# Kernel optimization log

Hardware: AMD Instinct MI355X
Metric: run time of the kernel (lower is better)

The kernel has to match this reference:

```python
import jax, jax.numpy as jnp
import numpy as np

NF = 256  # node_feat_size
GF = 256  # graph_feat_size
V = 262144
G = 4096


def setup_inputs() -> dict:
    key = jax.random.key(0)
    ks = jax.random.split(key, 12)
    node_feats = jax.random.normal(ks[0], (V, NF), dtype=jnp.float32)
    g_feats = jax.random.normal(ks[1], (G, GF), dtype=jnp.float32)
    segment_ids = jnp.sort(jax.random.randint(ks[2], (V,), 0, G, dtype=jnp.int32))
    s = 0.05
    # compute_logits: Linear(NF+GF -> 1)
    Wl = jax.random.normal(ks[3], (1, NF + GF), dtype=jnp.float32) * s
    bl = jnp.zeros((1,), dtype=jnp.float32)
    # project_nodes: Linear(NF -> GF)  (dropout=0 -> identity)
    Wp = jax.random.normal(ks[4], (GF, NF), dtype=jnp.float32) * s
    bp = jnp.zeros((GF,), dtype=jnp.float32)
    # GRUCell(GF, GF), torch gate order (r, z, n)
    W_ih = jax.random.normal(ks[5], (3 * GF, GF), dtype=jnp.float32) * s
    W_hh = jax.random.normal(ks[6], (3 * GF, GF), dtype=jnp.float32) * s
    b_ih = jnp.zeros((3 * GF,), dtype=jnp.float32)
    b_hh = jnp.zeros((3 * GF,), dtype=jnp.float32)
    return dict(node_feats=node_feats, g_feats=g_feats, segment_ids=segment_ids,
                Wl=Wl, bl=bl, Wp=Wp, bp=bp,
                W_ih=W_ih, W_hh=W_hh, b_ih=b_ih, b_hh=b_hh)


def reference(node_feats, g_feats, segment_ids, Wl, bl, Wp, bp, W_ih, W_hh, b_ih, b_hh):
    num_graphs = g_feats.shape[0]
    # broadcast relu(g_feats) to nodes, concat with node feats, logits Linear + LeakyReLU
    gb = jax.nn.relu(g_feats)[segment_ids]                      # [V, GF]
    cat = jnp.concatenate([gb, node_feats], axis=1)             # [V, GF+NF]
    z = jax.nn.leaky_relu(cat @ Wl.T + bl, negative_slope=0.01) # [V, 1]
    # segmented softmax over nodes per graph
    m = jax.ops.segment_max(z, segment_ids, num_segments=num_graphs,
                            indices_are_sorted=True)            # [G, 1]
    e = jnp.exp(z - m[segment_ids])                             # [V, 1]
    denom = jax.ops.segment_sum(e, segment_ids, num_segments=num_graphs,
                                indices_are_sorted=True)        # [G, 1]
    a = e / denom[segment_ids]                                  # [V, 1]
    # project nodes (dropout p=0 -> identity) and weighted sum per graph
    hv = node_feats @ Wp.T + bp                                 # [V, GF]
    context = jax.ops.segment_sum(a * hv, segment_ids, num_segments=num_graphs,
                                  indices_are_sorted=True)      # [G, GF]
    context = jax.nn.elu(context)
    # GRUCell: input=context, hidden=g_feats, torch gate order r,z,n
    gi = context @ W_ih.T + b_ih                                # [G, 3*GF]
    gh = g_feats @ W_hh.T + b_hh                                # [G, 3*GF]
    i_r, i_z, i_n = jnp.split(gi, 3, axis=1)
    h_r, h_z, h_n = jnp.split(gh, 3, axis=1)
    r = jax.nn.sigmoid(i_r + h_r)
    u = jax.nn.sigmoid(i_z + h_z)
    n = jnp.tanh(i_n + r * h_n)
    h_new = (1.0 - u) * n + u * g_feats
    return h_new
```

## Files before the change

### kernel.cpp

```cpp
#include <hip/hip_runtime.h>
#include <hip/hip_bf16.h>
#include <stdint.h>

typedef unsigned short u16;
typedef __attribute__((ext_vector_type(8))) short short8;
typedef __attribute__((ext_vector_type(4))) float floatx4;

#define NFEAT 256

__device__ __forceinline__ unsigned short f2b(float f) {
    unsigned int x = __builtin_bit_cast(unsigned int, f);
    x += 0x7fffu + ((x >> 16) & 1u);
    return (unsigned short)(x >> 16);
}
__device__ __forceinline__ float sigmoidf_(float x) {
    return 1.0f / (1.0f + __expf(-x));
}

__global__ void __launch_bounds__(256)
k0_prep(const int* __restrict__ seg, int V, int G, int* __restrict__ off,
        const float* __restrict__ Wp, const float* __restrict__ Wih,
        const float* __restrict__ Whh,
        u16* __restrict__ wpb, u16* __restrict__ wihb, u16* __restrict__ whhb)
{
    const int i = blockIdx.x * 256 + threadIdx.x;

    {
        const int n1 = 256 * 256;
        const int n2 = n1 + 768 * 256;
        const int n3 = n2 + 768 * 256;
        int idx = i * 2;
        if (idx < n3) {
            const float* src; u16* dst; int o;
            if (idx < n1)      { src = Wp;  dst = wpb;  o = idx; }
            else if (idx < n2) { src = Wih; dst = wihb; o = idx - n1; }
            else               { src = Whh; dst = whhb; o = idx - n2; }
            float2 v = *(const float2*)(src + o);
            dst[o]     = f2b(v.x);
            dst[o + 1] = f2b(v.y);
        }
    }

    if (i < V) {
        int s = seg[i];
        int prev = (i == 0) ? -1 : seg[i - 1];
        if (s != prev) {
            for (int g2 = prev + 1; g2 <= s; ++g2) off[g2] = i;
        }
        if (i == V - 1) {
            for (int g2 = s + 1; g2 <= G; ++g2) off[g2] = V;
        }
    }
}

__global__ void __launch_bounds__(256)
k1_attn_pool(const float* __restrict__ nf, const float* __restrict__ gf,
             const int* __restrict__ off, const float* __restrict__ Wl,
             const float* __restrict__ bl,
             u16* __restrict__ s_out,
             float* __restrict__ pres, u16* __restrict__ gfb)
{
    const int g = blockIdx.x;
    const int t = threadIdx.x;
    const int lane = t & 63;
    const int wv = t >> 6;
    __shared__ float red[4];
    __shared__ float accs[4][256];
    __shared__ float lws[4];

    const int start = off[g];
    const int count = off[g + 1] - start;

    const float* base = nf + (size_t)start * NFEAT + lane * 4;
    float4 x[4] = {{0,0,0,0},{0,0,0,0},{0,0,0,0},{0,0,0,0}};
    #pragma unroll
    for (int r = 0; r < 4; ++r) {
        int i = wv * 4 + r;
        if (i < count) x[r] = *(const float4*)(base + (size_t)i * NFEAT);
    }

    const float4 wn = *(const float4*)(Wl + NFEAT + lane * 4);

    const float gfv = gf[(size_t)g * NFEAT + t];
    gfb[(size_t)g * NFEAT + t] = f2b(gfv);
    float v = fmaxf(gfv, 0.0f) * Wl[t];
    #pragma unroll
    for (int o = 32; o > 0; o >>= 1) v += __shfl_xor(v, o);
    if (lane == 0) red[wv] = v;
    __syncthreads();
    const float gbase = (red[0] + red[1]) + (red[2] + red[3]) + bl[0];

    float l = 0.0f;
    float4 acc = {0.f, 0.f, 0.f, 0.f};
    for (int i = wv * 4; i < count; i += 16) {
        float4 nx[4] = {{0,0,0,0},{0,0,0,0},{0,0,0,0},{0,0,0,0}};
        #pragma unroll
        for (int r = 0; r < 4; ++r) {
            if (i + 16 + r < count) nx[r] = *(const float4*)(base + (size_t)(i + 16 + r) * NFEAT);
        }
        float d[4];
        #pragma unroll
        for (int r = 0; r < 4; ++r)
            d[r] = x[r].x * wn.x + x[r].y * wn.y + x[r].z * wn.z + x[r].w * wn.w;
        #pragma unroll
        for (int o = 32; o > 0; o >>= 1) {
            #pragma unroll
            for (int r = 0; r < 4; ++r) d[r] += __shfl_xor(d[r], o);
        }
        #pragma unroll
        for (int r = 0; r < 4; ++r) {
            float z = d[r] + gbase;
            z = (z > 0.0f) ? z : 0.01f * z;
            float p = (i + r < count) ? __expf(z) : 0.0f;
            l += p;
            acc.x += p * x[r].x;
            acc.y += p * x[r].y;
            acc.z += p * x[r].z;
            acc.w += p * x[r].w;
        }
        x[0] = nx[0]; x[1] = nx[1]; x[2] = nx[2]; x[3] = nx[3];
    }

    accs[wv][lane * 4 + 0] = acc.x;
    accs[wv][lane * 4 + 1] = acc.y;
    accs[wv][lane * 4 + 2] = acc.z;
    accs[wv][lane * 4 + 3] = acc.w;
    if (lane == 0) lws[wv] = l;
    __syncthreads();

    const float L = (lws[0] + lws[1]) + (lws[2] + lws[3]);
    const float sv = (accs[0][t] + accs[1][t]) + (accs[2][t] + accs[3][t]);
    const float inv = (L > 0.0f) ? 1.0f / L : 0.0f;
    s_out[(size_t)g * NFEAT + t] = f2b(sv * inv);
    if (t == 0) pres[g] = (count > 0) ? 1.0f : 0.0f;
}

#define CTX_LD 264
__global__ void __launch_bounds__(512)
k2_fused(const u16* __restrict__ s, const u16* __restrict__ wpb,
         const float* __restrict__ bp, const float* __restrict__ pres,
         const u16* __restrict__ gfb, const float* __restrict__ gf,
         const u16* __restrict__ wihb, const u16* __restrict__ whhb,
         const float* __restrict__ bih, const float* __restrict__ bhh,
         float* __restrict__ out)
{
    __shared__ u16 ctx[16][CTX_LD];
    const int t = threadIdx.x;
    const int w = t >> 6;
    const int lane = t & 63;
    const int m0 = blockIdx.x * 16;
    const int lr = lane & 15;
    const int kh = lane >> 4;

    {
        const short* A = (const short*)s + (size_t)(m0 + lr) * NFEAT + kh * 8;
        short8 af[8];
        #pragma unroll
        for (int kk = 0; kk < 8; ++kk) af[kk] = *(const short8*)(A + kk * 32);

        #pragma unroll
        for (int nt = 0; nt < 2; ++nt) {
            const int n0 = (w * 2 + nt) * 16;
            const short* B = (const short*)wpb + (size_t)(n0 + lr) * NFEAT + kh * 8;
            floatx4 acc = {0.f, 0.f, 0.f, 0.f};
            #pragma unroll
            for (int kk = 0; kk < 8; ++kk)
                acc = __builtin_amdgcn_mfma_f32_16x16x32_bf16(af[kk], *(const short8*)(B + kk * 32), acc, 0, 0, 0);
            const int col = n0 + lr;
            const float bias = bp[col];
            #pragma unroll
            for (int r = 0; r < 4; ++r) {
                int rl = kh * 4 + r;
                float x = acc[r] + bias * pres[m0 + rl];
                x = (x > 0.0f) ? x : (__expf(x) - 1.0f);
                ctx[rl][col] = f2b(x);
            }
        }
    }
    __syncthreads();

    short8 a1[8], a2[8];
    #pragma unroll
    for (int kk = 0; kk < 8; ++kk)
        a1[kk] = *(const short8*)&ctx[lr][kk * 32 + kh * 8];
    {
        const short* A2 = (const short*)gfb + (size_t)(m0 + lr) * NFEAT + kh * 8;
        #pragma unroll
        for (int kk = 0; kk < 8; ++kk) a2[kk] = *(const short8*)(A2 + kk * 32);
    }

    #pragma unroll
    for (int jt = 0; jt < 2; ++jt) {
        const int j0 = (w * 2 + jt) * 16;
        const size_t boff = (size_t)(j0 + lr) * NFEAT + kh * 8;
        const short* Bir = (const short*)wihb + boff;
        const short* Biz = Bir + 256 * NFEAT;
        const short* Bin = Bir + 512 * NFEAT;
        const short* Bhr = (const short*)whhb + boff;
        const short* Bhz = Bhr + 256 * NFEAT;
        const short* Bhn = Bhr + 512 * NFEAT;

        floatx4 air = {0,0,0,0}, aiz = {0,0,0,0}, ain = {0,0,0,0};
        floatx4 ahr = {0,0,0,0}, ahz = {0,0,0,0}, ahn = {0,0,0,0};
        #pragma unroll
        for (int kk = 0; kk < 8; ++kk) {
            const int k = kk * 32;
            air = __builtin_amdgcn_mfma_f32_16x16x32_bf16(a1[kk], *(const short8*)(Bir + k), air, 0, 0, 0);
            aiz = __builtin_amdgcn_mfma_f32_16x16x32_bf16(a1[kk], *(const short8*)(Biz + k), aiz, 0, 0, 0);
            ain = __builtin_amdgcn_mfma_f32_16x16x32_bf16(a1[kk], *(const short8*)(Bin + k), ain, 0, 0, 0);
            ahr = __builtin_amdgcn_mfma_f32_16x16x32_bf16(a2[kk], *(const short8*)(Bhr + k), ahr, 0, 0, 0);
            ahz = __builtin_amdgcn_mfma_f32_16x16x32_bf16(a2[kk], *(const short8*)(Bhz + k), ahz, 0, 0, 0);
            ahn = __builtin_amdgcn_mfma_f32_16x16x32_bf16(a2[kk], *(const short8*)(Bhn + k), ahn, 0, 0, 0);
        }
        const int col = j0 + lr;
        const float b_ir = bih[col], b_iz = bih[256 + col], b_in = bih[512 + col];
        const float b_hr = bhh[col], b_hz = bhh[256 + col], b_hn = bhh[512 + col];
        #pragma unroll
        for (int r = 0; r < 4; ++r) {
            int row = m0 + kh * 4 + r;
            float rg = sigmoidf_((air[r] + b_ir) + (ahr[r] + b_hr));
            float ug = sigmoidf_((aiz[r] + b_iz) + (ahz[r] + b_hz));
            float ng = tanhf((ain[r] + b_in) + rg * (ahn[r] + b_hn));
            float h  = gf[(size_t)row * NFEAT + col];
            out[(size_t)row * NFEAT + col] = (1.0f - ug) * ng + ug * h;
        }
    }
}

extern "C" void kernel_launch(void* const* d_in, const int* in_sizes, int n_in,
                              void* d_out, int out_size, void* d_ws, size_t ws_size,
                              hipStream_t stream)
{
    const float* nf  = (const float*)d_in[0];
    const float* gf  = (const float*)d_in[1];
    const int*   seg = (const int*)d_in[2];
    const float* Wl  = (const float*)d_in[3];
    const float* bl  = (const float*)d_in[4];
    const float* Wp  = (const float*)d_in[5];
    const float* bp  = (const float*)d_in[6];
    const float* Wih = (const float*)d_in[7];
    const float* Whh = (const float*)d_in[8];
    const float* bih = (const float*)d_in[9];
    const float* bhh = (const float*)d_in[10];

    const int V = in_sizes[2];
    const int G = in_sizes[1] / NFEAT;

    char* ws = (char*)d_ws;
    u16*   sbuf = (u16*)ws;                           ws += (size_t)G * NFEAT * 2;
    u16*   gfb  = (u16*)ws;                           ws += (size_t)G * NFEAT * 2;
    u16*   wpb  = (u16*)ws;                           ws += (size_t)256 * 256 * 2;
    u16*   wihb = (u16*)ws;                           ws += (size_t)768 * 256 * 2;
    u16*   whhb = (u16*)ws;                           ws += (size_t)768 * 256 * 2;
    float* pres = (float*)ws;                         ws += (size_t)G * 4;
    int*   off  = (int*)ws;                           ws += (size_t)(G + 1) * 4;

    k0_prep<<<(V + 255) / 256, 256, 0, stream>>>(seg, V, G, off, Wp, Wih, Whh,
                                                 wpb, wihb, whhb);
    k1_attn_pool<<<G, 256, 0, stream>>>(nf, gf, off, Wl, bl, sbuf, pres, gfb);
    k2_fused<<<G / 16, 512, 0, stream>>>(sbuf, wpb, bp, pres, gfb, gf,
                                         wihb, whhb, bih, bhh, (float*)d_out);
    (void)ws_size; (void)n_in; (void)out_size;
}
```

Measured before the change: 423.0 us.

## Fold prep kernel into attention pool with in-kernel segment search and row-per-quarter-wave loads

Removes the separate prep launch. Each block now finds its segment bounds with a wave-cooperative radix-32 ballot search over the sorted ids, and one wave per block converts a slice of the weight matrices to bf16. The node-feature loop is also restructured so each quarter-wave handles a whole row with 16-wide nontemporal loads, which shortens the dot-product shuffle reduction. The trade-offs are a per-block search of about four ballot rounds and extra cross-lane reductions at the end.

```diff
diff --git a/kernel.cpp b/kernel.cpp
--- a/kernel.cpp
+++ b/kernel.cpp
@@ -3,136 +3,162 @@
 #include <stdint.h>
 
 typedef unsigned short u16;
+typedef unsigned int   u32;
 typedef __attribute__((ext_vector_type(8))) short short8;
 typedef __attribute__((ext_vector_type(4))) float floatx4;
+typedef __attribute__((ext_vector_type(4))) float f4;
 
 #define NFEAT 256
-
-__device__ __forceinline__ unsigned short f2b(float f) {
-    unsigned int x = __builtin_bit_cast(unsigned int, f);
+#define WPAIRS 229376
+#define P_WP   32768
+#define P_WIH  131072
+
+__device__ __forceinline__ u16 f2b(float f) {
+    u32 x = __builtin_bit_cast(u32, f);
     x += 0x7fffu + ((x >> 16) & 1u);
-    return (unsigned short)(x >> 16);
+    return (u16)(x >> 16);
 }
 __device__ __forceinline__ float sigmoidf_(float x) {
     return 1.0f / (1.0f + __expf(-x));
 }
-
-__global__ void __launch_bounds__(256)
-k0_prep(const int* __restrict__ seg, int V, int G, int* __restrict__ off,
-        const float* __restrict__ Wp, const float* __restrict__ Wih,
-        const float* __restrict__ Whh,
-        u16* __restrict__ wpb, u16* __restrict__ wihb, u16* __restrict__ whhb)
-{
-    const int i = blockIdx.x * 256 + threadIdx.x;
-
-    {
-        const int n1 = 256 * 256;
-        const int n2 = n1 + 768 * 256;
-        const int n3 = n2 + 768 * 256;
-        int idx = i * 2;
-        if (idx < n3) {
-            const float* src; u16* dst; int o;
-            if (idx < n1)      { src = Wp;  dst = wpb;  o = idx; }
-            else if (idx < n2) { src = Wih; dst = wihb; o = idx - n1; }
-            else               { src = Whh; dst = whhb; o = idx - n2; }
-            float2 v = *(const float2*)(src + o);
-            dst[o]     = f2b(v.x);
-            dst[o + 1] = f2b(v.y);
-        }
-    }
-
-    if (i < V) {
-        int s = seg[i];
-        int prev = (i == 0) ? -1 : seg[i - 1];
-        if (s != prev) {
-            for (int g2 = prev + 1; g2 <= s; ++g2) off[g2] = i;
-        }
-        if (i == V - 1) {
-            for (int g2 = s + 1; g2 <= G; ++g2) off[g2] = V;
-        }
-    }
+__device__ __forceinline__ f4 ldnt4(const float* p) {
+    return __builtin_nontemporal_load((const f4*)p);
 }
 
 __global__ void __launch_bounds__(256)
 k1_attn_pool(const float* __restrict__ nf, const float* __restrict__ gf,
-             const int* __restrict__ off, const float* __restrict__ Wl,
-             const float* __restrict__ bl,
-             u16* __restrict__ s_out,
-             float* __restrict__ pres, u16* __restrict__ gfb)
+             const int* __restrict__ seg, int V, int G,
+             const float* __restrict__ Wl, const float* __restrict__ bl,
+             const float* __restrict__ Wp, const float* __restrict__ Wih,
+             const float* __restrict__ Whh,
+             u16* __restrict__ s_out, float* __restrict__ pres,
+             u16* __restrict__ gfb, u16* __restrict__ wpb,
+             u16* __restrict__ wihb, u16* __restrict__ whhb)
 {
-    const int g = blockIdx.x;
-    const int t = threadIdx.x;
+    const int g    = blockIdx.x;
+    const int t    = threadIdx.x;
     const int lane = t & 63;
-    const int wv = t >> 6;
-    __shared__ float red[4];
-    __shared__ float accs[4][256];
+    const int wv   = t >> 6;
+    const int sub  = lane & 15;
+    const int q    = lane >> 4;
+
+    __shared__ float sh_gbase;
+    __shared__ __align__(16) float accs[4][256];
     __shared__ float lws[4];
 
-    const int start = off[g];
-    const int count = off[g + 1] - start;
-
-    const float* base = nf + (size_t)start * NFEAT + lane * 4;
-    float4 x[4] = {{0,0,0,0},{0,0,0,0},{0,0,0,0},{0,0,0,0}};
-    #pragma unroll
-    for (int r = 0; r < 4; ++r) {
-        int i = wv * 4 + r;
-        if (i < count) x[r] = *(const float4*)(base + (size_t)i * NFEAT);
-    }
-
-    const float4 wn = *(const float4*)(Wl + NFEAT + lane * 4);
-
-    const float gfv = gf[(size_t)g * NFEAT + t];
-    gfb[(size_t)g * NFEAT + t] = f2b(gfv);
-    float v = fmaxf(gfv, 0.0f) * Wl[t];
-    #pragma unroll
-    for (int o = 32; o > 0; o >>= 1) v += __shfl_xor(v, o);
-    if (lane == 0) red[wv] = v;
+    const int h = lane >> 5;
+    const int target = g + h;
+    int S0 = 1;
+    while ((long long)S0 * 32 < V) S0 *= 32;
+    int pos = 0;
+    for (int step = S0; step >= 1; step /= 32) {
+        if (pos < V) {
+            int idx = pos + (lane & 31) * step + step - 1;
+            idx = min(idx, V - 1);
+            unsigned long long b = __ballot(seg[idx] < target);
+            int cnt = h ? __popcll(b >> 32) : __popcll(b & 0xFFFFFFFFull);
+            pos += cnt * step;
+        }
+    }
+    pos = min(pos, V);
+    const int start = __shfl(pos, 0);
+    const int end_  = __shfl(pos, 32);
+    const int count = end_ - start;
+
+    const float* rowbase = nf + (size_t)start * NFEAT + sub * 16;
+    const int r0 = wv * 4 + q;
+    f4 x[4] = {{0,0,0,0},{0,0,0,0},{0,0,0,0},{0,0,0,0}};
+    if (r0 < count) {
+        const float* p = rowbase + (size_t)r0 * NFEAT;
+        #pragma unroll
+        for (int j = 0; j < 4; ++j) x[j] = ldnt4(p + j * 4);
+    }
+    f4 wn[4];
+    #pragma unroll
+    for (int j = 0; j < 4; ++j) wn[j] = *(const f4*)(Wl + NFEAT + sub * 16 + j * 4);
+
+    if (wv == 0) {
+        f4 gv = *(const f4*)(gf + (size_t)g * NFEAT + lane * 4);
+        f4 wl = *(const f4*)(Wl + lane * 4);
+        float v = fmaxf(gv[0], 0.f) * wl[0] + fmaxf(gv[1], 0.f) * wl[1]
+                + fmaxf(gv[2], 0.f) * wl[2] + fmaxf(gv[3], 0.f) * wl[3];
+        #pragma unroll
+        for (int o = 32; o > 0; o >>= 1) v += __shfl_xor(v, o);
+        if (lane == 0) sh_gbase = v + bl[0];
+        uint2 pk;
+        pk.x = (u32)f2b(gv[0]) | ((u32)f2b(gv[1]) << 16);
+        pk.y = (u32)f2b(gv[2]) | ((u32)f2b(gv[3]) << 16);
+        *(uint2*)(gfb + (size_t)g * NFEAT + lane * 4) = pk;
+    } else if (wv == 1) {
+        const int PPB = (WPAIRS + G - 1) / G;
+        for (int pi = lane; pi < PPB; pi += 64) {
+            int P = g * PPB + pi;
+            if (P < WPAIRS) {
+                const float* src; u32* dst; int o;
+                if (P < P_WP)       { src = Wp;  dst = (u32*)wpb;  o = P; }
+                else if (P < P_WIH) { src = Wih; dst = (u32*)wihb; o = P - P_WP; }
+                else                { src = Whh; dst = (u32*)whhb; o = P - P_WIH; }
+                float2 v = *(const float2*)(src + (size_t)o * 2);
+                dst[o] = (u32)f2b(v.x) | ((u32)f2b(v.y) << 16);
+            }
+        }
+    }
     __syncthreads();
-    const float gbase = (red[0] + red[1]) + (red[2] + red[3]) + bl[0];
-
-    float l = 0.0f;
-    float4 acc = {0.f, 0.f, 0.f, 0.f};
+    const float gbase = sh_gbase;
+
+    float l = 0.f;
+    f4 acc[4] = {{0,0,0,0},{0,0,0,0},{0,0,0,0},{0,0,0,0}};
     for (int i = wv * 4; i < count; i += 16) {
-        float4 nx[4] = {{0,0,0,0},{0,0,0,0},{0,0,0,0},{0,0,0,0}};
-        #pragma unroll
-        for (int r = 0; r < 4; ++r) {
-            if (i + 16 + r < count) nx[r] = *(const float4*)(base + (size_t)(i + 16 + r) * NFEAT);
-        }
-        float d[4];
-        #pragma unroll
-        for (int r = 0; r < 4; ++r)
-            d[r] = x[r].x * wn.x + x[r].y * wn.y + x[r].z * wn.z + x[r].w * wn.w;
-        #pragma unroll
-        for (int o = 32; o > 0; o >>= 1) {
+        f4 nx[4] = {{0,0,0,0},{0,0,0,0},{0,0,0,0},{0,0,0,0}};
+        const int rn = i + 16 + q;
+        if (rn < count) {
+            const float* p = rowbase + (size_t)rn * NFEAT;
             #pragma unroll
-            for (int r = 0; r < 4; ++r) d[r] += __shfl_xor(d[r], o);
-        }
-        #pragma unroll
-        for (int r = 0; r < 4; ++r) {
-            float z = d[r] + gbase;
-            z = (z > 0.0f) ? z : 0.01f * z;
-            float p = (i + r < count) ? __expf(z) : 0.0f;
-            l += p;
-            acc.x += p * x[r].x;
-            acc.y += p * x[r].y;
-            acc.z += p * x[r].z;
-            acc.w += p * x[r].w;
-        }
+            for (int j = 0; j < 4; ++j) nx[j] = ldnt4(p + j * 4);
+        }
+        float d = 0.f;
+        #pragma unroll
+        for (int j = 0; j < 4; ++j)
+            d += x[j][0]*wn[j][0] + x[j][1]*wn[j][1]
+               + x[j][2]*wn[j][2] + x[j][3]*wn[j][3];
+        d += __shfl_xor(d, 1);
+        d += __shfl_xor(d, 2);
+        d += __shfl_xor(d, 4);
+        d += __shfl_xor(d, 8);
+        float z = d + gbase;
+        z = (z > 0.f) ? z : 0.01f * z;
+        float pw = (i + q < count) ? __expf(z) : 0.f;
+        l += pw;
+        #pragma unroll
+        for (int j = 0; j < 4; ++j) acc[j] += pw * x[j];
         x[0] = nx[0]; x[1] = nx[1]; x[2] = nx[2]; x[3] = nx[3];
     }
 
-    accs[wv][lane * 4 + 0] = acc.x;
-    accs[wv][lane * 4 + 1] = acc.y;
-    accs[wv][lane * 4 + 2] = acc.z;
-    accs[wv][lane * 4 + 3] = acc.w;
+    #pragma unroll
+    for (int j = 0; j < 4; ++j) {
+        #pragma unroll
+        for (int c = 0; c < 4; ++c) {
+            float v = acc[j][c];
+            v += __shfl_xor(v, 16);
+            v += __shfl_xor(v, 32);
+            acc[j][c] = v;
+        }
+    }
+    l += __shfl_xor(l, 16);
+    l += __shfl_xor(l, 32);
+    if (lane < 16) {
+        #pragma unroll
+        for (int j = 0; j < 4; ++j)
+            *(f4*)&accs[wv][sub * 16 + j * 4] = acc[j];
+    }
     if (lane == 0) lws[wv] = l;
     __syncthreads();
 
-    const float L = (lws[0] + lws[1]) + (lws[2] + lws[3]);
-    const float sv = (accs[0][t] + accs[1][t]) + (accs[2][t] + accs[3][t]);
-    const float inv = (L > 0.0f) ? 1.0f / L : 0.0f;
+    const float L   = (lws[0] + lws[1]) + (lws[2] + lws[3]);
+    const float sv  = (accs[0][t] + accs[1][t]) + (accs[2][t] + accs[3][t]);
+    const float inv = (L > 0.f) ? 1.f / L : 0.f;
     s_out[(size_t)g * NFEAT + t] = f2b(sv * inv);
-    if (t == 0) pres[g] = (count > 0) ? 1.0f : 0.0f;
+    if (t == 0) pres[g] = (count > 0) ? 1.f : 0.f;
 }
 
 #define CTX_LD 264
@@ -253,11 +279,10 @@
     u16*   wihb = (u16*)ws;                           ws += (size_t)768 * 256 * 2;
     u16*   whhb = (u16*)ws;                           ws += (size_t)768 * 256 * 2;
     float* pres = (float*)ws;                         ws += (size_t)G * 4;
-    int*   off  = (int*)ws;                           ws += (size_t)(G + 1) * 4;
-
-    k0_prep<<<(V + 255) / 256, 256, 0, stream>>>(seg, V, G, off, Wp, Wih, Whh,
-                                                 wpb, wihb, whhb);
-    k1_attn_pool<<<G, 256, 0, stream>>>(nf, gf, off, Wl, bl, sbuf, pres, gfb);
+
+    k1_attn_pool<<<G, 256, 0, stream>>>(nf, gf, seg, V, G, Wl, bl,
+                                        Wp, Wih, Whh,
+                                        sbuf, pres, gfb, wpb, wihb, whhb);
     k2_fused<<<G / 16, 512, 0, stream>>>(sbuf, wpb, bp, pres, gfb, gf,
                                          wihb, whhb, bih, bhh, (float*)d_out);
     (void)ws_size; (void)n_in; (void)out_size;
```

Measured after the change: 424.9 us. No clear change (+0.4%).
